# Kernel optimization log

Measured on AMD Instinct MI355X. Metric: run time of the kernel, lower is better.

The kernel has to match this reference:

```python
import jax, jax.numpy as jnp
import numpy as np

DIM = 3072
NUM_HEADS = 24
HEAD_DIM = DIM // NUM_HEADS  # 128
EPS = 1e-6


def rms_norm(x, scale):
    # x: (..., D); torch F.rms_norm over last dim
    var = jnp.mean(jnp.square(x), axis=-1, keepdims=True)
    return x * jax.lax.rsqrt(var + EPS) * scale


def apply_rope(xq, xk, freqs_cis):
    # xq, xk: (B, H, L, D); freqs_cis: (1, 1, L, D//2, 2, 2)
    B, H, L, D = xq.shape
    xq_ = xq.astype(jnp.float32).reshape(B, H, L, D // 2, 1, 2)
    xk_ = xk.astype(jnp.float32).reshape(B, H, L, D // 2, 1, 2)
    # (1,1,L,D/2,2) * (B,H,L,D/2,1) broadcast -> (B,H,L,D/2,2)
    xq_out = freqs_cis[..., 0] * xq_[..., 0] + freqs_cis[..., 1] * xq_[..., 1]
    xk_out = freqs_cis[..., 0] * xk_[..., 0] + freqs_cis[..., 1] * xk_[..., 1]
    return xq_out.reshape(B, H, L, D).astype(xq.dtype), xk_out.reshape(B, H, L, D).astype(xk.dtype)


def setup_inputs() -> dict:
    key = jax.random.key(0)
    ks = jax.random.split(key, 7)
    B, L = 1, 2048
    x = jax.random.normal(ks[0], (B, L, DIM), dtype=jnp.float32)
    pe = jax.random.normal(ks[1], (1, 1, L, HEAD_DIM // 2, 2, 2), dtype=jnp.float32)
    # parameters (torch nn.Linear layout: weight is (out, in))
    s = 1.0 / np.sqrt(DIM)
    w_qkv = jax.random.uniform(ks[2], (3 * DIM, DIM), minval=-s, maxval=s, dtype=jnp.float32)
    w_proj = jax.random.uniform(ks[3], (DIM, DIM), minval=-s, maxval=s, dtype=jnp.float32)
    b_proj = jax.random.uniform(ks[4], (DIM,), minval=-s, maxval=s, dtype=jnp.float32)
    q_scale = jnp.ones((HEAD_DIM,), dtype=jnp.float32)
    k_scale = jnp.ones((HEAD_DIM,), dtype=jnp.float32)
    return {"x": x, "pe": pe, "w_qkv": w_qkv, "w_proj": w_proj,
            "b_proj": b_proj, "q_scale": q_scale, "k_scale": k_scale}


def reference(x, pe, w_qkv, w_proj, b_proj, q_scale, k_scale):
    B, L, _ = x.shape
    qkv = x @ w_qkv.T  # (B, L, 3*DIM)
    qkv = qkv.reshape(B, L, 3, NUM_HEADS, HEAD_DIM)
    qkv = jnp.transpose(qkv, (2, 0, 3, 1, 4))  # (3, B, H, L, D)
    q, k, v = qkv[0], qkv[1], qkv[2]
    # QKNorm (RMSNorm over head_dim)
    q = rms_norm(q, q_scale)
    k = rms_norm(k, k_scale)
    # RoPE
    q, k = apply_rope(q, k, pe)
    # SDPA: softmax(q k^T / sqrt(D)) v, non-causal
    scores = jnp.einsum("bhqd,bhkd->bhqk", q, k) / np.sqrt(HEAD_DIM).astype(np.float32)
    attn = jax.nn.softmax(scores, axis=-1)
    out = jnp.einsum("bhqk,bhkd->bhqd", attn, v)  # (B, H, L, D)
    out = jnp.transpose(out, (0, 2, 1, 3)).reshape(B, L, DIM)  # B L (H D)
    return out @ w_proj.T + b_proj
```

## Files before the change

### kernel.cpp

```cpp
#include <hip/hip_runtime.h>
#include <hip/hip_bf16.h>

typedef _Float16 f16;
typedef _Float16 f16x2 __attribute__((ext_vector_type(2)));
typedef _Float16 f16x4 __attribute__((ext_vector_type(4)));
typedef _Float16 f16x8 __attribute__((ext_vector_type(8)));
typedef float f32x4 __attribute__((ext_vector_type(4)));

#define L_SEQ 2048
#define DIM 3072
#define NHEAD 24
#define HDIM 128

__device__ __forceinline__ void gll16(const f16* g, f16* l) {
    __builtin_amdgcn_global_load_lds((const __attribute__((address_space(1))) void*)g,
                                     (__attribute__((address_space(3))) void*)l, 16, 0, 0);
}

__global__ __launch_bounds__(256) void f32_to_f16_kernel(const float* __restrict__ s,
                                                         f16* __restrict__ d, int n4) {
    int i = blockIdx.x * blockDim.x + threadIdx.x;
    int stride = gridDim.x * blockDim.x;
    for (; i < n4; i += stride) {
        float4 v = reinterpret_cast<const float4*>(s)[i];
        f16x4 o = {(f16)v.x, (f16)v.y, (f16)v.z, (f16)v.w};
        reinterpret_cast<f16x4*>(d)[i] = o;
    }
}


#define GEMM_BODY(T, VM, DO_STAGE)                                                      \
    {                                                                                   \
        asm volatile("s_waitcnt vmcnt(" #VM ")" ::: "memory");                          \
        __builtin_amdgcn_s_barrier();                                                   \
        __builtin_amdgcn_sched_barrier(0);                                              \
        const int slot_ = (T) % 3;                                                      \
        f16x8 af[4], bf[4];                                                             \
        _Pragma("unroll") for (int i = 0; i < 4; i++)                                   \
            af[i] = *reinterpret_cast<const f16x8*>(                                    \
                &As[slot_][(wr + i * 16 + laneM) * 32 + fc16]);                         \
        _Pragma("unroll") for (int j = 0; j < 4; j++)                                   \
            bf[j] = *reinterpret_cast<const f16x8*>(                                    \
                &Bs[slot_][(wc + j * 16 + laneM) * 32 + fc16]);                         \
        if (DO_STAGE) {                                                                 \
            const int t2 = (T) + 2;                                                     \
            const int s2 = t2 % 3;                                                      \
            gll16(Asrc0 + t2 * 32, &As[s2][dstoff]);                                    \
            gll16(Asrc1 + t2 * 32, &As[s2][4096 + dstoff]);                             \
            gll16(Bsrc + t2 * 32, &Bs[s2][dstoff]);                                     \
        }                                                                               \
        __builtin_amdgcn_s_setprio(1);                                                  \
        _Pragma("unroll") for (int i = 0; i < 4; i++)                                   \
            _Pragma("unroll") for (int j = 0; j < 4; j++)                               \
                acc[i][j] =                                                             \
                    __builtin_amdgcn_mfma_f32_16x16x32_f16(af[i], bf[j], acc[i][j],     \
                                                           0, 0, 0);                    \
        __builtin_amdgcn_s_setprio(0);                                                  \
    }

template <int MODE>
__global__ __launch_bounds__(512, 4) void rg_gemm(const f16* __restrict__ A,
                                                  const f16* __restrict__ B,
                                                  f16* __restrict__ Cf16,
                                                  float* __restrict__ Cf32,
                                                  const float* __restrict__ bias,
                                                  int M, int N, int K) {
    __shared__ f16 As[3][256 * 32];
    __shared__ f16 Bs[3][128 * 32];
    const int tid = threadIdx.x;
    const int wid = tid >> 6;
    const int lane = tid & 63;
    const int grp = lane >> 4;
    const int laneM = lane & 15;

    const int nwg = gridDim.x * gridDim.y;
    const int orig = blockIdx.y * gridDim.x + blockIdx.x;
    const int wgid = (orig & 7) * (nwg >> 3) + (orig >> 3);
    const int bx = wgid % gridDim.x;
    const int by = wgid / gridDim.x;
    const int m0 = by * 256;
    const int n0 = bx * 128;

    const int wr = (wid >> 1) * 64;
    const int wc = (wid & 1) * 64;
    const int NT = K >> 5;
    const int fc16 = (grp ^ ((laneM >> 1) & 3)) * 8;

    const int srow = tid >> 2;
    const int scol = (((tid & 3) ^ ((tid >> 3) & 3)) << 3);
    const f16* Asrc0 = A + (size_t)(m0 + srow) * K + scol;
    const f16* Asrc1 = A + (size_t)(m0 + 128 + srow) * K + scol;
    const f16* Bsrc = B + (size_t)(n0 + srow) * K + scol;
    const int dstoff = wid * 512;

    const f32x4 vzero = {0.f, 0.f, 0.f, 0.f};
    f32x4 acc[4][4];
#pragma unroll
    for (int i = 0; i < 4; i++)
#pragma unroll
        for (int j = 0; j < 4; j++) acc[i][j] = vzero;

#pragma unroll
    for (int t = 0; t < 2; t++) {
        gll16(Asrc0 + t * 32, &As[t][dstoff]);
        gll16(Asrc1 + t * 32, &As[t][4096 + dstoff]);
        gll16(Bsrc + t * 32, &Bs[t][dstoff]);
    }

    int t = 0;
    for (; t < NT - 2; ++t) GEMM_BODY(t, 3, true);
    GEMM_BODY(t, 3, false); ++t;
    GEMM_BODY(t, 0, false);

#pragma unroll
    for (int i = 0; i < 4; i++)
#pragma unroll
        for (int j = 0; j < 4; j++)
#pragma unroll
            for (int r = 0; r < 4; r++) {
                int row = m0 + wr + i * 16 + grp * 4 + r;
                int col = n0 + wc + j * 16 + laneM;
                float v = acc[i][j][r];
                if (MODE == 0) {
                    Cf16[(size_t)row * N + col] = (f16)v;
                } else {
                    Cf32[(size_t)row * N + col] = v + bias[col];
                }
            }
}

__global__ __launch_bounds__(64) void fuse_qk_kernel(const f16* __restrict__ qkv,
                                                     const float* __restrict__ pe,
                                                     const float* __restrict__ qs,
                                                     const float* __restrict__ ks,
                                                     f16* __restrict__ qb,
                                                     f16* __restrict__ kb) {
    const int l = blockIdx.x;
    const int h = blockIdx.y;
    const int i = threadIdx.x;
    const f16* row = qkv + (size_t)l * (3 * DIM) + h * HDIM;
    f16x2 qp = *reinterpret_cast<const f16x2*>(row + 2 * i);
    f16x2 kp = *reinterpret_cast<const f16x2*>(row + DIM + 2 * i);
    float q0 = (float)qp[0], q1 = (float)qp[1];
    float k0 = (float)kp[0], k1 = (float)kp[1];
    float sq = q0 * q0 + q1 * q1;
    float sk = k0 * k0 + k1 * k1;
#pragma unroll
    for (int off = 1; off < 64; off <<= 1) {
        sq += __shfl_xor(sq, off);
        sk += __shfl_xor(sk, off);
    }
    const float SCALE = 0.08838834764831845f;
    float rq = rsqrtf(sq * (1.0f / 128.0f) + 1e-6f) * SCALE;
    float rk = rsqrtf(sk * (1.0f / 128.0f) + 1e-6f);
    float4 w = *reinterpret_cast<const float4*>(pe + ((size_t)l * 64 + i) * 4);
    float qa = q0 * rq * qs[2 * i];
    float qbv = q1 * rq * qs[2 * i + 1];
    float ka = k0 * rk * ks[2 * i];
    float kbv = k1 * rk * ks[2 * i + 1];
    f16x2 qo = {(f16)(w.x * qa + w.y * qbv), (f16)(w.z * qa + w.w * qbv)};
    f16x2 ko = {(f16)(w.x * ka + w.y * kbv), (f16)(w.z * ka + w.w * kbv)};
    *reinterpret_cast<f16x2*>(qb + ((size_t)h * L_SEQ + l) * HDIM + 2 * i) = qo;
    *reinterpret_cast<f16x2*>(kb + ((size_t)h * L_SEQ + l) * HDIM + 2 * i) = ko;
}

__global__ __launch_bounds__(256) void transpose_v_kernel(const f16* __restrict__ qkv,
                                                          f16* __restrict__ vT) {
    __shared__ f16 tile[32][33];
    const int tx = threadIdx.x & 31;
    const int ty = threadIdx.x >> 5;
    const int c0 = blockIdx.x * 32;
    const int r0 = blockIdx.y * 32;
#pragma unroll
    for (int j = 0; j < 4; j++)
        tile[ty + j * 8][tx] = qkv[(size_t)(r0 + ty + j * 8) * (3 * DIM) + 2 * DIM + c0 + tx];
    __syncthreads();
#pragma unroll
    for (int j = 0; j < 4; j++)
        vT[(size_t)(c0 + ty + j * 8) * L_SEQ + r0 + tx] = tile[tx][ty + j * 8];
}

#define KVBLK 64
#define NSTEP (L_SEQ / KVBLK)

__device__ __forceinline__ void stage_kv(const f16* __restrict__ Kh,
                                         const f16* __restrict__ Vh,
                                         int k0, f16* Kt, f16* Vt, int tid) {
    const int wid = tid >> 6;
    const int krow = tid >> 4;
    const int kcl = (tid & 15) ^ (krow & 7);
    const int vrow = tid >> 3;
    const int vcl = (tid & 7) ^ (vrow & 7);
#pragma unroll
    for (int i = 0; i < 4; i++)
        gll16(Kh + (size_t)(k0 + i * 16 + krow) * HDIM + kcl * 8, Kt + i * 2048 + wid * 512);
#pragma unroll
    for (int i = 0; i < 4; i++)
        gll16(Vh + (size_t)(i * 32 + vrow) * L_SEQ + k0 + vcl * 8, Vt + i * 2048 + wid * 512);
}

__global__ __launch_bounds__(256, 2) void attn_kernel(const f16* __restrict__ qb,
                                                      const f16* __restrict__ kb,
                                                      const f16* __restrict__ vT,
                                                      f16* __restrict__ attnb) {
    __shared__ f16 Kt[2][64 * 128];
    __shared__ f16 Vt[2][128 * 64];
    __shared__ f16 Pl[4][16 * 72];
    const int tid = threadIdx.x;
    const int wid = tid >> 6;
    const int lane = tid & 63;
    const int grp = lane >> 4;
    const int laneM = lane & 15;
    const int h = blockIdx.y;
    const int q0 = blockIdx.x * 64 + wid * 16;
    const f16* Qh = qb + (size_t)h * L_SEQ * HDIM;
    const f16* Kh = kb + (size_t)h * L_SEQ * HDIM;
    const f16* Vh = vT + (size_t)h * HDIM * L_SEQ;

    f16x8 qf[4];
#pragma unroll
    for (int c = 0; c < 4; c++)
        qf[c] = *reinterpret_cast<const f16x8*>(Qh + (size_t)(q0 + laneM) * HDIM + c * 32 + grp * 8);

    const f32x4 vzero = {0.f, 0.f, 0.f, 0.f};
    f32x4 O[8];
#pragma unroll
    for (int f = 0; f < 8; f++) O[f] = vzero;
    float m = -3.0e38f;
    float lsum = 0.f;
    f16* Prow = &Pl[wid][laneM * 72];
    const int swz = laneM & 7;

    stage_kv(Kh, Vh, 0, Kt[0], Vt[0], tid);

    for (int step = 0; step < NSTEP; ++step) {
        const int cur = step & 1;
        __syncthreads();
        if (step + 1 < NSTEP)
            stage_kv(Kh, Vh, (step + 1) * KVBLK, Kt[cur ^ 1], Vt[cur ^ 1], tid);
        const f16* Kc = Kt[cur];
        const f16* Vc = Vt[cur];

        f32x4 s[4];
#pragma unroll
        for (int cc = 0; cc < 4; cc++) s[cc] = vzero;
#pragma unroll
        for (int cc = 0; cc < 4; cc++) {
            f16x8 kf[4];
#pragma unroll
            for (int c = 0; c < 4; c++)
                kf[c] = *reinterpret_cast<const f16x8*>(
                    &Kc[(cc * 16 + laneM) * 128 + (((c * 4 + grp) ^ swz) * 8)]);
#pragma unroll
            for (int c = 0; c < 4; c++)
                s[cc] = __builtin_amdgcn_mfma_f32_16x16x32_f16(kf[c], qf[c], s[cc], 0, 0, 0);
        }

        float pmax = s[0][0];
#pragma unroll
        for (int cc = 0; cc < 4; cc++)
#pragma unroll
            for (int r = 0; r < 4; r++) pmax = fmaxf(pmax, s[cc][r]);
        if (!__all(pmax <= m + 8.0f)) {
            float pm = fmaxf(pmax, __shfl_xor(pmax, 16));
            pm = fmaxf(pm, __shfl_xor(pm, 32));
            float mnew = fmaxf(m, pm);
            float alpha = __expf(m - mnew);
            m = mnew;
            lsum *= alpha;
            float af[4];
#pragma unroll
            for (int r = 0; r < 4; r++) af[r] = __shfl(alpha, grp * 4 + r);
#pragma unroll
            for (int f = 0; f < 8; f++)
#pragma unroll
                for (int r = 0; r < 4; r++) O[f][r] *= af[r];
        }
        float ps = 0.f;
#pragma unroll
        for (int cc = 0; cc < 4; cc++) {
            f16x4 pk;
#pragma unroll
            for (int r = 0; r < 4; r++) {
                float p = __expf(s[cc][r] - m);
                ps += p;
                pk[r] = (f16)p;
            }
            *reinterpret_cast<f16x4*>(Prow + cc * 16 + grp * 4) = pk;
        }
        ps += __shfl_xor(ps, 16);
        ps += __shfl_xor(ps, 32);
        lsum += ps;

#pragma unroll
        for (int z = 0; z < 2; z++) {
            f16x8 pa = *reinterpret_cast<const f16x8*>(Prow + z * 32 + grp * 8);
#pragma unroll
            for (int f = 0; f < 8; f++) {
                f16x8 vf = *reinterpret_cast<const f16x8*>(
                    &Vc[(f * 16 + laneM) * 64 + (((z * 4 + grp) ^ swz) * 8)]);
                O[f] = __builtin_amdgcn_mfma_f32_16x16x32_f16(pa, vf, O[f], 0, 0, 0);
            }
        }
    }

    float li = 1.0f / lsum;
    float lf[4];
#pragma unroll
    for (int r = 0; r < 4; r++) lf[r] = __shfl(li, grp * 4 + r);
#pragma unroll
    for (int f = 0; f < 8; f++)
#pragma unroll
        for (int r = 0; r < 4; r++) {
            int row = q0 + grp * 4 + r;
            attnb[(size_t)row * DIM + h * HDIM + f * 16 + laneM] = (f16)(O[f][r] * lf[r]);
        }
}

extern "C" void kernel_launch(void* const* d_in, const int* in_sizes, int n_in,
                              void* d_out, int out_size, void* d_ws, size_t ws_size,
                              hipStream_t stream) {
    const float* x = (const float*)d_in[0];
    const float* pe = (const float*)d_in[1];
    const float* w_qkv = (const float*)d_in[2];
    const float* w_proj = (const float*)d_in[3];
    const float* b_proj = (const float*)d_in[4];
    const float* q_scale = (const float*)d_in[5];
    const float* k_scale = (const float*)d_in[6];
    float* out = (float*)d_out;

    char* ws = (char*)d_ws;
    f16* xb     = (f16*)(ws + 0);
    f16* wqkvb  = (f16*)(ws + 12582912);
    f16* wprojb = (f16*)(ws + 69206016);
    f16* qkvb   = (f16*)(ws + 88080384);
    f16* qbuf   = (f16*)(ws + 125829120);
    f16* kbuf   = (f16*)(ws + 138412032);
    f16* vT     = (f16*)(ws + 150994944);
    f16* attnb  = (f16*)(ws + 163577856);
    if (ws_size < 176160768) return;

    f32_to_f16_kernel<<<1024, 256, 0, stream>>>(x, xb, (2048 * 3072) / 4);
    f32_to_f16_kernel<<<2048, 256, 0, stream>>>(w_qkv, wqkvb, (9216 * 3072) / 4);
    f32_to_f16_kernel<<<1024, 256, 0, stream>>>(w_proj, wprojb, (3072 * 3072) / 4);

    rg_gemm<0><<<dim3(72, 8), 512, 0, stream>>>(xb, wqkvb, qkvb, nullptr, nullptr,
                                                2048, 9216, 3072);
    fuse_qk_kernel<<<dim3(2048, 24), 64, 0, stream>>>(qkvb, pe, q_scale, k_scale, qbuf, kbuf);
    transpose_v_kernel<<<dim3(96, 64), 256, 0, stream>>>(qkvb, vT);
    attn_kernel<<<dim3(32, 24), 256, 0, stream>>>(qbuf, kbuf, vT, attnb);
    rg_gemm<1><<<dim3(24, 8), 512, 0, stream>>>(attnb, wprojb, nullptr, out, b_proj,
                                                2048, 3072, 3072);
}
```

Measured before the change: 392.4 us.

## Use smaller-tile triple-buffered GEMM for output projection

Adds a new GEMM kernel with 128x128 tiles, 256 threads and a three-slot LDS ring, and uses it for the output projection in place of the larger-tile 512-thread GEMM. The grid grows from 192 to 384 workgroups, which is meant to fill the GPU's compute units better, while loads are issued two steps ahead of compute and the workgroup order is remapped. In exchange, each workgroup reuses less data, so global and LDS traffic per flop goes up.

```diff
diff --git a/kernel.cpp b/kernel.cpp
--- a/kernel.cpp
+++ b/kernel.cpp
@@ -129,6 +129,108 @@
             }
 }
 
+
+#define GEMM_BODY_S(T, VM, DO_STAGE)                                                    \
+    {                                                                                   \
+        asm volatile("s_waitcnt vmcnt(" #VM ")" ::: "memory");                          \
+        __builtin_amdgcn_s_barrier();                                                   \
+        __builtin_amdgcn_sched_barrier(0);                                              \
+        const int slot_ = (T) % 3;                                                      \
+        f16x8 af[4], bf[4];                                                             \
+        _Pragma("unroll") for (int i = 0; i < 4; i++)                                   \
+            af[i] = *reinterpret_cast<const f16x8*>(                                    \
+                &As[slot_][(wr + i * 16 + laneM) * 32 + fc16]);                         \
+        _Pragma("unroll") for (int j = 0; j < 4; j++)                                   \
+            bf[j] = *reinterpret_cast<const f16x8*>(                                    \
+                &Bs[slot_][(wc + j * 16 + laneM) * 32 + fc16]);                         \
+        if (DO_STAGE) {                                                                 \
+            const int t2 = (T) + 2;                                                     \
+            const int s2 = t2 % 3;                                                      \
+            gll16(Asrc + t2 * 32, &As[s2][dstoff]);                                     \
+            gll16(Asrc + (size_t)64 * K + t2 * 32, &As[s2][2048 + dstoff]);             \
+            gll16(Bsrc + t2 * 32, &Bs[s2][dstoff]);                                     \
+            gll16(Bsrc + (size_t)64 * K + t2 * 32, &Bs[s2][2048 + dstoff]);             \
+        }                                                                               \
+        __builtin_amdgcn_s_setprio(1);                                                  \
+        _Pragma("unroll") for (int i = 0; i < 4; i++)                                   \
+            _Pragma("unroll") for (int j = 0; j < 4; j++)                               \
+                acc[i][j] =                                                             \
+                    __builtin_amdgcn_mfma_f32_16x16x32_f16(af[i], bf[j], acc[i][j],     \
+                                                           0, 0, 0);                    \
+        __builtin_amdgcn_s_setprio(0);                                                  \
+    }
+
+template <int MODE>
+__global__ __launch_bounds__(256, 4) void rg_gemm_s(const f16* __restrict__ A,
+                                                    const f16* __restrict__ B,
+                                                    f16* __restrict__ Cf16,
+                                                    float* __restrict__ Cf32,
+                                                    const float* __restrict__ bias,
+                                                    int M, int N, int K) {
+    __shared__ f16 As[3][128 * 32];
+    __shared__ f16 Bs[3][128 * 32];
+    const int tid = threadIdx.x;
+    const int wid = tid >> 6;
+    const int lane = tid & 63;
+    const int grp = lane >> 4;
+    const int laneM = lane & 15;
+
+    const int nwg = gridDim.x * gridDim.y;
+    const int orig = blockIdx.y * gridDim.x + blockIdx.x;
+    const int wgid = (orig & 7) * (nwg >> 3) + (orig >> 3);
+    const int bx = wgid % gridDim.x;
+    const int by = wgid / gridDim.x;
+    const int m0 = by * 128;
+    const int n0 = bx * 128;
+
+    const int wr = (wid >> 1) * 64;
+    const int wc = (wid & 1) * 64;
+    const int NT = K >> 5;
+    const int fc16 = (grp ^ ((laneM >> 1) & 3)) * 8;
+
+    const int srow = tid >> 2;
+    const int scol = (((tid & 3) ^ ((tid >> 3) & 3)) << 3);
+    const f16* Asrc = A + (size_t)(m0 + srow) * K + scol;
+    const f16* Bsrc = B + (size_t)(n0 + srow) * K + scol;
+    const int dstoff = wid * 512;
+
+    const f32x4 vzero = {0.f, 0.f, 0.f, 0.f};
+    f32x4 acc[4][4];
+#pragma unroll
+    for (int i = 0; i < 4; i++)
+#pragma unroll
+        for (int j = 0; j < 4; j++) acc[i][j] = vzero;
+
+#pragma unroll
+    for (int t = 0; t < 2; t++) {
+        gll16(Asrc + t * 32, &As[t][dstoff]);
+        gll16(Asrc + (size_t)64 * K + t * 32, &As[t][2048 + dstoff]);
+        gll16(Bsrc + t * 32, &Bs[t][dstoff]);
+        gll16(Bsrc + (size_t)64 * K + t * 32, &Bs[t][2048 + dstoff]);
+    }
+
+    int t = 0;
+    for (; t < NT - 2; ++t) GEMM_BODY_S(t, 4, true);
+    GEMM_BODY_S(t, 4, false); ++t;
+    GEMM_BODY_S(t, 0, false);
+
+#pragma unroll
+    for (int i = 0; i < 4; i++)
+#pragma unroll
+        for (int j = 0; j < 4; j++)
+#pragma unroll
+            for (int r = 0; r < 4; r++) {
+                int row = m0 + wr + i * 16 + grp * 4 + r;
+                int col = n0 + wc + j * 16 + laneM;
+                float v = acc[i][j][r];
+                if (MODE == 0) {
+                    Cf16[(size_t)row * N + col] = (f16)v;
+                } else {
+                    Cf32[(size_t)row * N + col] = v + bias[col];
+                }
+            }
+}
+
 __global__ __launch_bounds__(64) void fuse_qk_kernel(const f16* __restrict__ qkv,
                                                      const float* __restrict__ pe,
                                                      const float* __restrict__ qs,
@@ -349,6 +451,6 @@
     fuse_qk_kernel<<<dim3(2048, 24), 64, 0, stream>>>(qkvb, pe, q_scale, k_scale, qbuf, kbuf);
     transpose_v_kernel<<<dim3(96, 64), 256, 0, stream>>>(qkvb, vT);
     attn_kernel<<<dim3(32, 24), 256, 0, stream>>>(qbuf, kbuf, vT, attnb);
-    rg_gemm<1><<<dim3(24, 8), 512, 0, stream>>>(attnb, wprojb, nullptr, out, b_proj,
-                                                2048, 3072, 3072);
-}
+    rg_gemm_s<1><<<dim3(24, 16), 256, 0, stream>>>(attnb, wprojb, nullptr, out, b_proj,
+                                                   2048, 3072, 3072);
+}
```

Measured after the change: 386.7 us. About the same (-1.4%).

## Restructure GEMM into two-phase ping-pong with K=64 tiles

Applied to the files above, without the earlier changes.

The GEMM k-step grows from 32 to 64 with a matching 8-way XOR swizzle. Each k-step is split into two half-phases: the LDS fragment reads and global-to-LDS staging for one half are interleaved with MFMA work on the other, separated by extra barriers. Shared memory per block doubles, so launch bounds drop from 4 to 2 blocks per CU. The aim is better overlap of memory and matrix-core work and fewer loop iterations, at the cost of lower occupancy and more barriers.

```diff
diff --git a/kernel.cpp b/kernel.cpp
--- a/kernel.cpp
+++ b/kernel.cpp
@@ -29,44 +29,75 @@
 }
 
 
-#define GEMM_BODY(T, VM, DO_STAGE)                                                      \
+#define PH_BODY(T, VM, DO_STAGE)                                                        \
     {                                                                                   \
+        const int slot_ = (T) % 3;                                                      \
+        const int s2_ = ((T) + 2) % 3;                                                  \
+        const f16* Asl = &As[slot_][0];                                                 \
+        const f16* Bsl = &Bs[slot_][0];                                                 \
+                        \
         asm volatile("s_waitcnt vmcnt(" #VM ")" ::: "memory");                          \
         __builtin_amdgcn_s_barrier();                                                   \
         __builtin_amdgcn_sched_barrier(0);                                              \
-        const int slot_ = (T) % 3;                                                      \
-        f16x8 af[4], bf[4];                                                             \
-        _Pragma("unroll") for (int i = 0; i < 4; i++)                                   \
-            af[i] = *reinterpret_cast<const f16x8*>(                                    \
-                &As[slot_][(wr + i * 16 + laneM) * 32 + fc16]);                         \
+                             \
+        f16x8 bf[4][2], af[2][2];                                                       \
         _Pragma("unroll") for (int j = 0; j < 4; j++)                                   \
-            bf[j] = *reinterpret_cast<const f16x8*>(                                    \
-                &Bs[slot_][(wc + j * 16 + laneM) * 32 + fc16]);                         \
+            _Pragma("unroll") for (int kk = 0; kk < 2; kk++)                            \
+                bf[j][kk] = *reinterpret_cast<const f16x8*>(                            \
+                    &Bsl[(wc + j * 16 + laneM) * 64 + (((kk << 2) + grp) ^ swz8) * 8]); \
+        _Pragma("unroll") for (int u = 0; u < 2; u++)                                   \
+            _Pragma("unroll") for (int kk = 0; kk < 2; kk++)                            \
+                af[u][kk] = *reinterpret_cast<const f16x8*>(                            \
+                    &Asl[(wr + u * 16 + laneM) * 64 + (((kk << 2) + grp) ^ swz8) * 8]); \
         if (DO_STAGE) {                                                                 \
-            const int t2 = (T) + 2;                                                     \
-            const int s2 = t2 % 3;                                                      \
-            gll16(Asrc0 + t2 * 32, &As[s2][dstoff]);                                    \
-            gll16(Asrc1 + t2 * 32, &As[s2][4096 + dstoff]);                             \
-            gll16(Bsrc + t2 * 32, &Bs[s2][dstoff]);                                     \
+            _Pragma("unroll") for (int i = 0; i < 3; i++)                               \
+                gll16(AsrcP + (size_t)(i * 64) * K + ((T) + 2) * 64,                    \
+                      &As[s2_][i * 4096 + dstoff]);                                     \
         }                                                                               \
+        __builtin_amdgcn_s_barrier();                                                   \
+        __builtin_amdgcn_sched_barrier(0);                                              \
         __builtin_amdgcn_s_setprio(1);                                                  \
-        _Pragma("unroll") for (int i = 0; i < 4; i++)                                   \
+        _Pragma("unroll") for (int u = 0; u < 2; u++)                                   \
             _Pragma("unroll") for (int j = 0; j < 4; j++)                               \
-                acc[i][j] =                                                             \
-                    __builtin_amdgcn_mfma_f32_16x16x32_f16(af[i], bf[j], acc[i][j],     \
-                                                           0, 0, 0);                    \
+                _Pragma("unroll") for (int kk = 0; kk < 2; kk++)                        \
+                    acc[u][j] = __builtin_amdgcn_mfma_f32_16x16x32_f16(                 \
+                        af[u][kk], bf[j][kk], acc[u][j], 0, 0, 0);                      \
         __builtin_amdgcn_s_setprio(0);                                                  \
+        __builtin_amdgcn_s_barrier();                                                   \
+        __builtin_amdgcn_sched_barrier(0);                                              \
+                                             \
+        _Pragma("unroll") for (int u = 0; u < 2; u++)                                   \
+            _Pragma("unroll") for (int kk = 0; kk < 2; kk++)                            \
+                af[u][kk] = *reinterpret_cast<const f16x8*>(                            \
+                    &Asl[(wr + 32 + u * 16 + laneM) * 64 +                              \
+                         (((kk << 2) + grp) ^ swz8) * 8]);                              \
+        if (DO_STAGE) {                                                                 \
+            gll16(AsrcP + (size_t)(3 * 64) * K + ((T) + 2) * 64,                        \
+                  &As[s2_][3 * 4096 + dstoff]);                                         \
+            _Pragma("unroll") for (int i = 0; i < 2; i++)                               \
+                gll16(BsrcP + (size_t)(i * 64) * K + ((T) + 2) * 64,                    \
+                      &Bs[s2_][i * 4096 + dstoff]);                                     \
+        }                                                                               \
+        __builtin_amdgcn_s_barrier();                                                   \
+        __builtin_amdgcn_sched_barrier(0);                                              \
+        __builtin_amdgcn_s_setprio(1);                                                  \
+        _Pragma("unroll") for (int u = 0; u < 2; u++)                                   \
+            _Pragma("unroll") for (int j = 0; j < 4; j++)                               \
+                _Pragma("unroll") for (int kk = 0; kk < 2; kk++)                        \
+                    acc[2 + u][j] = __builtin_amdgcn_mfma_f32_16x16x32_f16(             \
+                        af[u][kk], bf[j][kk], acc[2 + u][j], 0, 0, 0);                  \
+        __builtin_amdgcn_s_setprio(0);                                                  \
     }
 
 template <int MODE>
-__global__ __launch_bounds__(512, 4) void rg_gemm(const f16* __restrict__ A,
+__global__ __launch_bounds__(512, 2) void ph_gemm(const f16* __restrict__ A,
                                                   const f16* __restrict__ B,
                                                   f16* __restrict__ Cf16,
                                                   float* __restrict__ Cf32,
                                                   const float* __restrict__ bias,
                                                   int M, int N, int K) {
-    __shared__ f16 As[3][256 * 32];
-    __shared__ f16 Bs[3][128 * 32];
+    __shared__ f16 As[3][256 * 64];
+    __shared__ f16 Bs[3][128 * 64];
     const int tid = threadIdx.x;
     const int wid = tid >> 6;
     const int lane = tid & 63;
@@ -83,14 +114,12 @@
 
     const int wr = (wid >> 1) * 64;
     const int wc = (wid & 1) * 64;
-    const int NT = K >> 5;
-    const int fc16 = (grp ^ ((laneM >> 1) & 3)) * 8;
-
-    const int srow = tid >> 2;
-    const int scol = (((tid & 3) ^ ((tid >> 3) & 3)) << 3);
-    const f16* Asrc0 = A + (size_t)(m0 + srow) * K + scol;
-    const f16* Asrc1 = A + (size_t)(m0 + 128 + srow) * K + scol;
-    const f16* Bsrc = B + (size_t)(n0 + srow) * K + scol;
+    const int NT = K >> 6;
+    const int swz8 = laneM & 7;
+
+    const int sg8 = (((tid & 7) ^ ((tid >> 3) & 7)) << 3);
+    const f16* AsrcP = A + (size_t)(m0 + (tid >> 3)) * K + sg8;
+    const f16* BsrcP = B + (size_t)(n0 + (tid >> 3)) * K + sg8;
     const int dstoff = wid * 512;
 
     const f32x4 vzero = {0.f, 0.f, 0.f, 0.f};
@@ -102,15 +131,18 @@
 
 #pragma unroll
     for (int t = 0; t < 2; t++) {
-        gll16(Asrc0 + t * 32, &As[t][dstoff]);
-        gll16(Asrc1 + t * 32, &As[t][4096 + dstoff]);
-        gll16(Bsrc + t * 32, &Bs[t][dstoff]);
+#pragma unroll
+        for (int i = 0; i < 4; i++)
+            gll16(AsrcP + (size_t)(i * 64) * K + t * 64, &As[t][i * 4096 + dstoff]);
+#pragma unroll
+        for (int i = 0; i < 2; i++)
+            gll16(BsrcP + (size_t)(i * 64) * K + t * 64, &Bs[t][i * 4096 + dstoff]);
     }
 
     int t = 0;
-    for (; t < NT - 2; ++t) GEMM_BODY(t, 3, true);
-    GEMM_BODY(t, 3, false); ++t;
-    GEMM_BODY(t, 0, false);
+    for (; t < NT - 2; ++t) PH_BODY(t, 6, true);
+    PH_BODY(t, 6, false); ++t;
+    PH_BODY(t, 0, false);
 
 #pragma unroll
     for (int i = 0; i < 4; i++)
@@ -344,11 +376,11 @@
     f32_to_f16_kernel<<<2048, 256, 0, stream>>>(w_qkv, wqkvb, (9216 * 3072) / 4);
     f32_to_f16_kernel<<<1024, 256, 0, stream>>>(w_proj, wprojb, (3072 * 3072) / 4);
 
-    rg_gemm<0><<<dim3(72, 8), 512, 0, stream>>>(xb, wqkvb, qkvb, nullptr, nullptr,
+    ph_gemm<0><<<dim3(72, 8), 512, 0, stream>>>(xb, wqkvb, qkvb, nullptr, nullptr,
                                                 2048, 9216, 3072);
     fuse_qk_kernel<<<dim3(2048, 24), 64, 0, stream>>>(qkvb, pe, q_scale, k_scale, qbuf, kbuf);
     transpose_v_kernel<<<dim3(96, 64), 256, 0, stream>>>(qkvb, vT);
     attn_kernel<<<dim3(32, 24), 256, 0, stream>>>(qbuf, kbuf, vT, attnb);
-    rg_gemm<1><<<dim3(24, 8), 512, 0, stream>>>(attnb, wprojb, nullptr, out, b_proj,
+    ph_gemm<1><<<dim3(24, 8), 512, 0, stream>>>(attnb, wprojb, nullptr, out, b_proj,
                                                 2048, 3072, 3072);
 }
```

After: 377.1 us. 1.04x faster.

## Split-K the output projection GEMM and batch heads in QK fuse kernel

Applied to the files above, without the earlier changes.

The output projection GEMM previously launched only 192 workgroups, so it runs as a 3-way split-K over K=3072, writing fp32 partials to reused workspace regions. A separate kernel then sums the three partials and adds the bias. The tile swizzle now walks the M dimension first, and the QK norm/RoPE kernel packs four heads per 256-thread block. Split-K raises occupancy on the device but adds extra fp32 partial traffic and another kernel launch. The partials overwrite earlier workspace buffers (xb, wqkvb, qkvb) that must be dead by then.

```diff
diff --git a/kernel.cpp b/kernel.cpp
--- a/kernel.cpp
+++ b/kernel.cpp
@@ -76,8 +76,8 @@
     const int nwg = gridDim.x * gridDim.y;
     const int orig = blockIdx.y * gridDim.x + blockIdx.x;
     const int wgid = (orig & 7) * (nwg >> 3) + (orig >> 3);
-    const int bx = wgid % gridDim.x;
-    const int by = wgid / gridDim.x;
+    const int by = wgid % gridDim.y;
+    const int bx = wgid / gridDim.y;
     const int m0 = by * 256;
     const int n0 = bx * 128;
 
@@ -129,15 +129,107 @@
             }
 }
 
-__global__ __launch_bounds__(64) void fuse_qk_kernel(const f16* __restrict__ qkv,
-                                                     const float* __restrict__ pe,
-                                                     const float* __restrict__ qs,
-                                                     const float* __restrict__ ks,
-                                                     f16* __restrict__ qb,
-                                                     f16* __restrict__ kb) {
+__global__ __launch_bounds__(512, 4) void rg_gemm_sk(const f16* __restrict__ A,
+                                                     const f16* __restrict__ B,
+                                                     float* __restrict__ P0,
+                                                     float* __restrict__ P1,
+                                                     float* __restrict__ P2,
+                                                     int M, int N, int K) {
+    __shared__ f16 As[3][256 * 32];
+    __shared__ f16 Bs[3][128 * 32];
+    const int tid = threadIdx.x;
+    const int wid = tid >> 6;
+    const int lane = tid & 63;
+    const int grp = lane >> 4;
+    const int laneM = lane & 15;
+
+    const int gxy = gridDim.x * gridDim.y;
+    const int nwg = gxy * gridDim.z;
+    const int orig = (blockIdx.z * gridDim.y + blockIdx.y) * gridDim.x + blockIdx.x;
+    const int wgid = (orig & 7) * (nwg >> 3) + (orig >> 3);
+    const int bz = wgid / gxy;
+    const int rem = wgid % gxy;
+    const int by = rem % gridDim.y;
+    const int bx = rem / gridDim.y;
+    const int m0 = by * 256;
+    const int n0 = bx * 128;
+    const int kbase = bz * 1024;
+    float* __restrict__ P = (bz == 0) ? P0 : (bz == 1) ? P1 : P2;
+
+    const int wr = (wid >> 1) * 64;
+    const int wc = (wid & 1) * 64;
+    const int NT = 32;
+    const int fc16 = (grp ^ ((laneM >> 1) & 3)) * 8;
+
+    const int srow = tid >> 2;
+    const int scol = (((tid & 3) ^ ((tid >> 3) & 3)) << 3);
+    const f16* Asrc0 = A + (size_t)(m0 + srow) * K + kbase + scol;
+    const f16* Asrc1 = A + (size_t)(m0 + 128 + srow) * K + kbase + scol;
+    const f16* Bsrc = B + (size_t)(n0 + srow) * K + kbase + scol;
+    const int dstoff = wid * 512;
+
+    const f32x4 vzero = {0.f, 0.f, 0.f, 0.f};
+    f32x4 acc[4][4];
+#pragma unroll
+    for (int i = 0; i < 4; i++)
+#pragma unroll
+        for (int j = 0; j < 4; j++) acc[i][j] = vzero;
+
+#pragma unroll
+    for (int t = 0; t < 2; t++) {
+        gll16(Asrc0 + t * 32, &As[t][dstoff]);
+        gll16(Asrc1 + t * 32, &As[t][4096 + dstoff]);
+        gll16(Bsrc + t * 32, &Bs[t][dstoff]);
+    }
+
+    int t = 0;
+    for (; t < NT - 2; ++t) GEMM_BODY(t, 3, true);
+    GEMM_BODY(t, 3, false); ++t;
+    GEMM_BODY(t, 0, false);
+
+#pragma unroll
+    for (int i = 0; i < 4; i++)
+#pragma unroll
+        for (int j = 0; j < 4; j++)
+#pragma unroll
+            for (int r = 0; r < 4; r++) {
+                int row = m0 + wr + i * 16 + grp * 4 + r;
+                int col = n0 + wc + j * 16 + laneM;
+                P[(size_t)row * N + col] = acc[i][j][r];
+            }
+}
+
+__global__ __launch_bounds__(256) void reduce3_bias_kernel(const float* __restrict__ p0,
+                                                           const float* __restrict__ p1,
+                                                           const float* __restrict__ p2,
+                                                           const float* __restrict__ bias,
+                                                           float* __restrict__ out) {
+    const int n4 = L_SEQ * DIM / 4;
+    int i = blockIdx.x * blockDim.x + threadIdx.x;
+    int stride = gridDim.x * blockDim.x;
+    for (; i < n4; i += stride) {
+        float4 a = reinterpret_cast<const float4*>(p0)[i];
+        float4 b = reinterpret_cast<const float4*>(p1)[i];
+        float4 c = reinterpret_cast<const float4*>(p2)[i];
+        float4 d = reinterpret_cast<const float4*>(bias)[i % (DIM / 4)];
+        float4 o;
+        o.x = a.x + b.x + c.x + d.x;
+        o.y = a.y + b.y + c.y + d.y;
+        o.z = a.z + b.z + c.z + d.z;
+        o.w = a.w + b.w + c.w + d.w;
+        reinterpret_cast<float4*>(out)[i] = o;
+    }
+}
+
+__global__ __launch_bounds__(256) void fuse_qk_kernel(const f16* __restrict__ qkv,
+                                                      const float* __restrict__ pe,
+                                                      const float* __restrict__ qs,
+                                                      const float* __restrict__ ks,
+                                                      f16* __restrict__ qb,
+                                                      f16* __restrict__ kb) {
     const int l = blockIdx.x;
-    const int h = blockIdx.y;
-    const int i = threadIdx.x;
+    const int h = blockIdx.y * 4 + (threadIdx.x >> 6);
+    const int i = threadIdx.x & 63;
     const f16* row = qkv + (size_t)l * (3 * DIM) + h * HDIM;
     f16x2 qp = *reinterpret_cast<const f16x2*>(row + 2 * i);
     f16x2 kp = *reinterpret_cast<const f16x2*>(row + DIM + 2 * i);
@@ -338,6 +430,9 @@
     f16* kbuf   = (f16*)(ws + 138412032);
     f16* vT     = (f16*)(ws + 150994944);
     f16* attnb  = (f16*)(ws + 163577856);
+    float* p0 = (float*)(ws + 0);
+    float* p1 = (float*)(ws + 25165824);
+    float* p2 = (float*)(ws + 88080384);
     if (ws_size < 176160768) return;
 
     f32_to_f16_kernel<<<1024, 256, 0, stream>>>(x, xb, (2048 * 3072) / 4);
@@ -346,9 +441,10 @@
 
     rg_gemm<0><<<dim3(72, 8), 512, 0, stream>>>(xb, wqkvb, qkvb, nullptr, nullptr,
                                                 2048, 9216, 3072);
-    fuse_qk_kernel<<<dim3(2048, 24), 64, 0, stream>>>(qkvb, pe, q_scale, k_scale, qbuf, kbuf);
+    fuse_qk_kernel<<<dim3(2048, 6), 256, 0, stream>>>(qkvb, pe, q_scale, k_scale, qbuf, kbuf);
     transpose_v_kernel<<<dim3(96, 64), 256, 0, stream>>>(qkvb, vT);
     attn_kernel<<<dim3(32, 24), 256, 0, stream>>>(qbuf, kbuf, vT, attnb);
-    rg_gemm<1><<<dim3(24, 8), 512, 0, stream>>>(attnb, wprojb, nullptr, out, b_proj,
-                                                2048, 3072, 3072);
-}
+    rg_gemm_sk<<<dim3(24, 8, 3), 512, 0, stream>>>(attnb, wprojb, p0, p1, p2,
+                                                   2048, 3072, 3072);
+    reduce3_bias_kernel<<<2048, 256, 0, stream>>>(p0, p1, p2, b_proj, out);
+}
```

Measured after the change: 402.8 us. +2.7%, slower.
